# Kernel tuning notes

Hardware: AMD Instinct MI355X
Metric: run time of the kernel (lower is better)

## Reference

```python
import jax, jax.numpy as jnp
import numpy as np
from functools import partial

T, B, CH, H, W = 16, 4, 128, 128, 128
TAU, VTH, ALPHA, EPS = 2.0, 1.0, 2.0, 1e-5

# ATan surrogate-gradient spike (spikingjelly surrogate.ATan, alpha=2.0)
@jax.custom_vjp
def spike(x):
    return (x >= 0.0).astype(x.dtype)

def _spike_fwd(x):
    return spike(x), x

def _spike_bwd(x, g):
    return (g * (ALPHA / 2.0) / (1.0 + (jnp.pi / 2.0 * ALPHA * x) ** 2),)

spike.defvjp(_spike_fwd, _spike_bwd)

def _conv(x, w):  # x [N,C,H,W], w [O,I,3,3], padding=1 -> SAME
    return jax.lax.conv_general_dilated(x, w, (1, 1), 'SAME',
                                        dimension_numbers=('NCHW', 'OIHW', 'NCHW'))

def _bn(x, g, b, m, v):  # inference-mode BatchNorm2d, channel axis 1
    inv = g / jnp.sqrt(v + EPS)
    return x * inv[:, None, None] + (b - m * inv)[:, None, None]

def _pool(x):  # MaxPool2d(2,2), NCHW
    return jax.lax.reduce_window(x, -jnp.inf, jax.lax.max,
                                 (1, 1, 2, 2), (1, 1, 2, 2), 'VALID')

def _lif(xs):  # xs [T, ...]; LIFNode: tau=2, v_th=1, v_reset=0, decay_input, hard reset (detached)
    def step(v, x):
        v = v + (x - v) / TAU                      # charge
        s = spike(v - VTH)                         # fire (Heaviside fwd, ATan bwd)
        v = v * (1.0 - jax.lax.stop_gradient(s))   # detached hard reset to 0
        return v, s
    return jax.lax.scan(step, jnp.zeros_like(xs[0]), xs)[1]

def _block(xs, w, g, b, m, v):  # conv -> BN -> LIF -> maxpool, xs [T,B,C,H,W]
    t, bs = xs.shape[0], xs.shape[1]
    y = _bn(_conv(xs.reshape((t * bs,) + xs.shape[2:]), w), g, b, m, v)
    y = _lif(y.reshape((t, bs) + y.shape[1:]))
    y = _pool(y.reshape((t * bs,) + y.shape[2:]))
    return y.reshape((t, bs) + y.shape[1:])


def setup_inputs() -> dict:
    key = jax.random.key(0)
    ks = jax.random.split(key, 8)
    inp = {'x': jax.random.uniform(ks[0], (T, B, 2, H, W), jnp.float32)}
    fan_ins = [2 * 9, CH * 9, CH * 9, CH * 9]
    for i in range(4):
        cin = 2 if i == 0 else CH
        inp[f'w{i+1}'] = jax.random.normal(ks[i + 1], (CH, cin, 3, 3), jnp.float32) * np.sqrt(2.0 / fan_ins[i]).astype(np.float32)
        inp[f'g{i+1}'] = jnp.ones((CH,), jnp.float32)
        inp[f'b{i+1}'] = jnp.zeros((CH,), jnp.float32)
        inp[f'm{i+1}'] = jnp.zeros((CH,), jnp.float32)
        inp[f'v{i+1}'] = jnp.ones((CH,), jnp.float32)
    inp['wfc'] = jax.random.normal(ks[5], (10, CH * 8 * 8), jnp.float32) * np.sqrt(1.0 / (CH * 64)).astype(np.float32)
    inp['bfc'] = jnp.zeros((10,), jnp.float32)
    return inp


def reference(x, w1, g1, b1, m1, v1, w2, g2, b2, m2, v2,
              w3, g3, b3, m3, v3, w4, g4, b4, m4, v4, wfc, bfc):
    y = _block(x, w1, g1, b1, m1, v1)   # [T,B,CH,64,64]
    y = _block(y, w2, g2, b2, m2, v2)   # [T,B,CH,32,32]
    y = _block(y, w3, g3, b3, m3, v3)   # [T,B,CH,16,16]
    y = _block(y, w4, g4, b4, m4, v4)   # [T,B,CH,8,8]
    z = y.reshape(y.shape[0], y.shape[1], -1) @ wfc.T + bfc  # [T,B,10]
    return _lif(z)                       # output spike train [T,B,10]
```

## Files before the change

### kernel.cpp

```cpp
#include <hip/hip_runtime.h>
#include <hip/hip_bf16.h>
#include <math.h>

#define T_STEPS 16

typedef __attribute__((ext_vector_type(8))) short bf16x8;
typedef __attribute__((ext_vector_type(16))) float f32x16;

__global__ __launch_bounds__(256) void prep_w3_kernel(
    const float* __restrict__ w2, const float* __restrict__ w3,
    const float* __restrict__ w4, __hip_bfloat16* __restrict__ wp2,
    __hip_bfloat16* __restrict__ wp3, __hip_bfloat16* __restrict__ wp4) {
  const float* w = blockIdx.y == 0 ? w2 : (blockIdx.y == 1 ? w3 : w4);
  __hip_bfloat16* wp = blockIdx.y == 0 ? wp2 : (blockIdx.y == 1 ? wp3 : wp4);
  int idx = blockIdx.x * 256 + threadIdx.x;
  if (idx >= 147456) return;
  int co = idx / 1152, rem = idx - co * 1152;
  int ci = rem / 9, tap = rem - ci * 9;
  float x = w[idx];
  float h = (float)__float2bfloat16(x);
  float r1 = x - h;
  float m = (float)__float2bfloat16(r1);
  float r2 = r1 - m;
  size_t base = (((size_t)tap * 16 + (ci >> 3)) * 128 + co) * 8 + (ci & 7);
  const size_t SSZ = 147456;
  wp[base] = __float2bfloat16(h);
  wp[SSZ + base] = __float2bfloat16(m);
  wp[2 * SSZ + base] = __float2bfloat16(r2);
}

__global__ __launch_bounds__(192) void pad_x_kernel(const float* __restrict__ x,
                                                    float* __restrict__ xp) {
  const int plane = blockIdx.x;
  const int row = blockIdx.y;
  const int c = threadIdx.x;
  if (c < 132) {
    float v = 0.f;
    int gr = row - 1, gc = c - 1;
    if ((unsigned)gr < 128u && (unsigned)gc < 128u)
      v = x[(size_t)plane * 16384 + gr * 128 + gc];
    xp[((size_t)plane * 130 + row) * 132 + c] = v;
  }
}

__global__ __launch_bounds__(256) void layer1_kernel(
    const float* __restrict__ xp, const float* __restrict__ w,
    const float* __restrict__ gn, const float* __restrict__ bn,
    const float* __restrict__ mn, const float* __restrict__ vn,
    __hip_bfloat16* __restrict__ out) {
  const int tid = threadIdx.x;
  const int tile = blockIdx.x;
  const int ty0 = (tile >> 2) * 32, tx0 = (tile & 3) * 32;
  const int co0 = blockIdx.y * 4;
  const int b = blockIdx.z;
  const int qx2 = (tid & 15) * 2;
  const int qy2 = (tid >> 4) * 2;
  const int yq = ty0 + qy2;
  const int xq = tx0 + qx2;

  float wreg[2][9][4];
#pragma unroll
  for (int j = 0; j < 4; ++j)
#pragma unroll
    for (int ci = 0; ci < 2; ++ci)
#pragma unroll
      for (int tap = 0; tap < 9; ++tap)
        wreg[ci][tap][j] = w[(co0 + j) * 18 + ci * 9 + tap];

  float scale[4], shift[4];
#pragma unroll
  for (int j = 0; j < 4; ++j) {
    float inv = gn[co0 + j] / sqrtf(vn[co0 + j] + 1e-5f);
    scale[j] = inv;
    shift[j] = bn[co0 + j] - mn[co0 + j] * inv;
  }

  float vm[4][4];
#pragma unroll
  for (int j = 0; j < 4; ++j)
#pragma unroll
    for (int p = 0; p < 4; ++p) vm[j][p] = 0.f;

  for (int t = 0; t < T_STEPS; ++t) {
    const float* xpt = xp + (size_t)((t * 4 + b) * 2) * 17160;
    float iv[2][4][4];
#pragma unroll
    for (int ci = 0; ci < 2; ++ci)
#pragma unroll
      for (int r = 0; r < 4; ++r)
        *(float4*)&iv[ci][r][0] =
            *(const float4*)(xpt + (size_t)(ci * 130 + yq + r) * 132 + xq);

    float acc[4][4];
#pragma unroll
    for (int j = 0; j < 4; ++j)
#pragma unroll
      for (int p = 0; p < 4; ++p) acc[j][p] = 0.f;

#pragma unroll
    for (int ci = 0; ci < 2; ++ci)
#pragma unroll
      for (int tap = 0; tap < 9; ++tap) {
        const int dy = tap / 3, dx = tap - dy * 3;
#pragma unroll
        for (int sy = 0; sy < 2; ++sy)
#pragma unroll
          for (int sx = 0; sx < 2; ++sx) {
            float xin = iv[ci][sy + dy][sx + dx];
            acc[0][sy * 2 + sx] += wreg[ci][tap][0] * xin;
            acc[1][sy * 2 + sx] += wreg[ci][tap][1] * xin;
            acc[2][sy * 2 + sx] += wreg[ci][tap][2] * xin;
            acc[3][sy * 2 + sx] += wreg[ci][tap][3] * xin;
          }
      }

    const int py = (ty0 >> 1) + (tid >> 4);
    const int px = (tx0 >> 1) + (tid & 15);
    short4 pk;
    short* pks = (short*)&pk;
#pragma unroll
    for (int j = 0; j < 4; ++j) {
      float mx = -1e30f;
#pragma unroll
      for (int p = 0; p < 4; ++p) {
        float yv = acc[j][p] * scale[j] + shift[j];
        float nv = vm[j][p] + (yv - vm[j][p]) * 0.5f;
        mx = fmaxf(mx, nv);
        vm[j][p] = (nv >= 1.0f) ? 0.f : nv;
      }
      __hip_bfloat16 bv = __float2bfloat16(mx >= 1.0f ? 1.0f : 0.0f);
      pks[j] = *(short*)&bv;
    }
    *(short4*)(out + (((size_t)(t * 4 + b) * 64 + py) * 64 + px) * 128 + co0) = pk;
  }
}

template <int S>
__global__ __launch_bounds__(256) void conv32_tb2_kernel(
    const __hip_bfloat16* __restrict__ spk, const __hip_bfloat16* __restrict__ wp,
    float* __restrict__ pre, int tb_base) {
  constexpr int TILES_X = S / 8;
  const int tile = blockIdx.x;
  const int ty0 = (tile / TILES_X) * 16;
  const int tx0 = (tile % TILES_X) * 8;
  const int pair = blockIdx.z;
  const int tbl0 = pair * 2;
  const int tb0 = tb_base + tbl0;
  const int tid = threadIdx.x;
  const int lane = tid & 63;
  const int wv = tid >> 6;

  __shared__ uint4 At4[2][2880];

#pragma unroll
  for (int i = 0; i < 2; ++i) {
    const __hip_bfloat16* sp = spk + (size_t)(tb0 + i) * S * S * 128;
    for (int job = tid; job < 2880; job += 256) {
      int c8 = job & 15, r = job >> 4;
      int y = (r * 6554) >> 16;
      int xx = r - y * 10;
      int gy = ty0 - 1 + y, gx = tx0 - 1 + xx;
      uint4 v = make_uint4(0u, 0u, 0u, 0u);
      if ((unsigned)gy < (unsigned)S && (unsigned)gx < (unsigned)S)
        v = *(const uint4*)(sp + ((size_t)(gy * S + gx)) * 128 + c8 * 8);
      At4[i][(y * 10 + xx) * 16 + (c8 ^ (xx & 7))] = v;
    }
  }
  __syncthreads();

  const int l31 = lane & 31, hh = lane >> 5;
  const int co = wv * 32 + l31;
  const int ly = l31 >> 3, lx = lane & 7;
  const uint4* A0 = &At4[0][0];
  const uint4* A1 = &At4[1][0];

  f32x16 acc0[4], acc1[4];
#pragma unroll
  for (int m = 0; m < 4; ++m)
#pragma unroll
    for (int r = 0; r < 16; ++r) { acc0[m][r] = 0.f; acc1[m][r] = 0.f; }

  const short* wpb = (const short*)wp + (size_t)co * 8;

  for (int tap = 0; tap < 9; ++tap) {
    const int dy = tap / 3, dx = tap - dy * 3;
    const int xx = lx + dx;
    const int sx7 = xx & 7;
#pragma unroll
    for (int kk = 0; kk < 8; ++kk) {
      const int kc = kk * 2 + hh;
      bf16x8 a0[4], a1[4];
#pragma unroll
      for (int m = 0; m < 4; ++m) {
        const int slot = ((m * 4 + ly + dy) * 10 + xx) * 16 + (kc ^ sx7);
        a0[m] = *(const bf16x8*)(A0 + slot);
        a1[m] = *(const bf16x8*)(A1 + slot);
      }
#pragma unroll
      for (int s = 0; s < 3; ++s) {
        bf16x8 bfr = *(const bf16x8*)(wpb + ((size_t)(s * 9 + tap) * 16 + kc) * 1024);
#pragma unroll
        for (int m = 0; m < 4; ++m)
          acc0[m] = __builtin_amdgcn_mfma_f32_32x32x16_bf16(a0[m], bfr, acc0[m], 0, 0, 0);
#pragma unroll
        for (int m = 0; m < 4; ++m)
          acc1[m] = __builtin_amdgcn_mfma_f32_32x32x16_bf16(a1[m], bfr, acc1[m], 0, 0, 0);
      }
    }
  }

  float* po0 = pre + (size_t)tbl0 * S * S * 128 + co;
  float* po1 = pre + (size_t)(tbl0 + 1) * S * S * 128 + co;
#pragma unroll
  for (int m = 0; m < 4; ++m)
#pragma unroll
    for (int r = 0; r < 16; ++r) {
      int row = (r & 3) + 8 * (r >> 2) + 4 * hh;
      int p = m * 32 + row;
      size_t off = ((size_t)(ty0 + (p >> 3)) * S + tx0 + (p & 7)) * 128;
      po0[off] = acc0[m][r];
      po1[off] = acc1[m][r];
    }
}

template <int S>
__global__ __launch_bounds__(256) void conv32_kernel(
    const __hip_bfloat16* __restrict__ spk, const __hip_bfloat16* __restrict__ wp,
    float* __restrict__ pre, int t_base) {
  constexpr int TILES_X = S / 8;
  const int tile = blockIdx.x;
  const int ty0 = (tile / TILES_X) * 16;
  const int tx0 = (tile % TILES_X) * 8;
  const int tbl = blockIdx.z;
  const int tbg = t_base * 4 + tbl;
  const int tid = threadIdx.x;
  const int lane = tid & 63;
  const int wv = tid >> 6;

  __shared__ uint4 At4[2880];

  const __hip_bfloat16* sp = spk + (size_t)tbg * S * S * 128;
#pragma unroll
  for (int k = 0; k < 12; ++k) {
    int job = k * 256 + tid;
    if (job < 2880) {
      int c8 = job & 15, r = job >> 4;
      int y = (r * 6554) >> 16;
      int xx = r - y * 10;
      int gy = ty0 - 1 + y, gx = tx0 - 1 + xx;
      uint4 v = make_uint4(0u, 0u, 0u, 0u);
      if ((unsigned)gy < (unsigned)S && (unsigned)gx < (unsigned)S)
        v = *(const uint4*)(sp + ((size_t)(gy * S + gx)) * 128 + c8 * 8);
      At4[(y * 10 + xx) * 16 + (c8 ^ (xx & 7))] = v;
    }
  }
  __syncthreads();

  const int l31 = lane & 31, hh = lane >> 5;
  const int co = wv * 32 + l31;
  const int ly = l31 >> 3, lx = lane & 7;

  f32x16 acc[4];
#pragma unroll
  for (int m = 0; m < 4; ++m)
#pragma unroll
    for (int r = 0; r < 16; ++r) acc[m][r] = 0.f;

  const short* wpb = (const short*)wp + (size_t)co * 8;

  for (int tap = 0; tap < 9; ++tap) {
    const int dy = tap / 3, dx = tap - dy * 3;
    const int xx = lx + dx;
    const int sx7 = xx & 7;
#pragma unroll
    for (int kk = 0; kk < 8; ++kk) {
      const int kc = kk * 2 + hh;
      bf16x8 a[4];
#pragma unroll
      for (int m = 0; m < 4; ++m)
        a[m] = *(const bf16x8*)(At4 + ((m * 4 + ly + dy) * 10 + xx) * 16 + (kc ^ sx7));
#pragma unroll
      for (int s = 0; s < 3; ++s) {
        bf16x8 bfr = *(const bf16x8*)(wpb + ((size_t)(s * 9 + tap) * 16 + kc) * 1024);
#pragma unroll
        for (int m = 0; m < 4; ++m)
          acc[m] = __builtin_amdgcn_mfma_f32_32x32x16_bf16(a[m], bfr, acc[m], 0, 0, 0);
      }
    }
  }

  float* po = pre + (size_t)tbl * S * S * 128 + co;
#pragma unroll
  for (int m = 0; m < 4; ++m)
#pragma unroll
    for (int r = 0; r < 16; ++r) {
      int row = (r & 3) + 8 * (r >> 2) + 4 * hh;
      int p = m * 32 + row;
      po[((size_t)(ty0 + (p >> 3)) * S + tx0 + (p & 7)) * 128] = acc[m][r];
    }
}

template <int S>
__global__ __launch_bounds__(256) void lif_pool_kernel(
    const float* __restrict__ pre, __hip_bfloat16* __restrict__ spk,
    float* __restrict__ vm, const float* __restrict__ gn,
    const float* __restrict__ bn, const float* __restrict__ mn,
    const float* __restrict__ vn, int t_base, int nt) {
  constexpr int OS = S / 2, NQ = OS * OS;
  const int tid = threadIdx.x;
  const int co = tid & 127;
  const int q = blockIdx.x * 2 + (tid >> 7);
  const int b = blockIdx.z;
  const int qy = q / OS, qx = q - qy * OS;
  float inv = gn[co] / sqrtf(vn[co] + 1e-5f);
  float sc = inv, sh = bn[co] - mn[co] * inv;
  float* vp = vm + (((size_t)b * NQ + q) * 4) * 128 + co;
  float v0, v1, v2, v3;
  if (t_base == 0) {
    v0 = v1 = v2 = v3 = 0.f;
  } else {
    v0 = vp[0]; v1 = vp[128]; v2 = vp[256]; v3 = vp[384];
  }
  const size_t rowstride = (size_t)S * 128;
  for (int t = 0; t < nt; ++t) {
    const float* p = pre + (((size_t)(t * 4 + b) * S + qy * 2) * S + qx * 2) * 128 + co;
    float x00 = p[0] * sc + sh;
    float x01 = p[128] * sc + sh;
    float x10 = p[rowstride] * sc + sh;
    float x11 = p[rowstride + 128] * sc + sh;
    float n0 = v0 + (x00 - v0) * 0.5f; float s0 = n0 >= 1.f ? 1.f : 0.f; v0 = n0 >= 1.f ? 0.f : n0;
    float n1 = v1 + (x01 - v1) * 0.5f; float s1 = n1 >= 1.f ? 1.f : 0.f; v1 = n1 >= 1.f ? 0.f : n1;
    float n2 = v2 + (x10 - v2) * 0.5f; float s2 = n2 >= 1.f ? 1.f : 0.f; v2 = n2 >= 1.f ? 0.f : n2;
    float n3 = v3 + (x11 - v3) * 0.5f; float s3 = n3 >= 1.f ? 1.f : 0.f; v3 = n3 >= 1.f ? 0.f : n3;
    float pooled = fmaxf(fmaxf(s0, s1), fmaxf(s2, s3));
    spk[((size_t)((t_base + t) * 4 + b) * NQ + q) * 128 + co] = __float2bfloat16(pooled);
  }
  if (t_base + nt < T_STEPS) {
    vp[0] = v0; vp[128] = v1; vp[256] = v2; vp[384] = v3;
  }
}

__global__ __launch_bounds__(256) void fc_kernel(const __hip_bfloat16* __restrict__ a4,
                                                 const float* __restrict__ wfc,
                                                 const float* __restrict__ bfc,
                                                 float* __restrict__ z) {
  const int tb = blockIdx.x;
  const int tid = threadIdx.x;
  const __hip_bfloat16* a = a4 + (size_t)tb * 8192;
  float part[10];
#pragma unroll
  for (int o = 0; o < 10; ++o) part[o] = 0.f;
  for (int i = tid; i < 8192; i += 256) {
    int co = i >> 6, yx = i & 63;
    float av = __bfloat162float(a[yx * 128 + co]);
#pragma unroll
    for (int o = 0; o < 10; ++o) part[o] += av * wfc[o * 8192 + i];
  }
#pragma unroll
  for (int o = 0; o < 10; ++o)
    for (int off = 32; off > 0; off >>= 1) part[o] += __shfl_xor(part[o], off, 64);
  __shared__ float red[4][10];
  if ((tid & 63) == 0) {
#pragma unroll
    for (int o = 0; o < 10; ++o) red[tid >> 6][o] = part[o];
  }
  __syncthreads();
  if (tid < 10)
    z[tb * 10 + tid] = red[0][tid] + red[1][tid] + red[2][tid] + red[3][tid] + bfc[tid];
}

__global__ void out_lif_kernel(const float* __restrict__ z, float* __restrict__ out) {
  int i = threadIdx.x;
  if (i < 40) {
    float v = 0.f;
    for (int t = 0; t < T_STEPS; ++t) {
      float yv = z[t * 40 + i];
      float nv = v + (yv - v) * 0.5f;
      float s = (nv >= 1.0f) ? 1.0f : 0.0f;
      out[t * 40 + i] = s;
      v = (nv >= 1.0f) ? 0.f : nv;
    }
  }
}

extern "C" void kernel_launch(void* const* d_in, const int* in_sizes, int n_in,
                              void* d_out, int out_size, void* d_ws, size_t ws_size,
                              hipStream_t stream) {
  const float* x = (const float*)d_in[0];
  const float* w1 = (const float*)d_in[1];
  const float* g1 = (const float*)d_in[2];
  const float* b1 = (const float*)d_in[3];
  const float* m1 = (const float*)d_in[4];
  const float* v1 = (const float*)d_in[5];
  const float* w2 = (const float*)d_in[6];
  const float* g2 = (const float*)d_in[7];
  const float* b2 = (const float*)d_in[8];
  const float* m2 = (const float*)d_in[9];
  const float* v2 = (const float*)d_in[10];
  const float* w3 = (const float*)d_in[11];
  const float* g3 = (const float*)d_in[12];
  const float* b3 = (const float*)d_in[13];
  const float* m3 = (const float*)d_in[14];
  const float* v3 = (const float*)d_in[15];
  const float* w4 = (const float*)d_in[16];
  const float* g4 = (const float*)d_in[17];
  const float* b4 = (const float*)d_in[18];
  const float* m4 = (const float*)d_in[19];
  const float* v4 = (const float*)d_in[20];
  const float* wfc = (const float*)d_in[21];
  const float* bfc = (const float*)d_in[22];
  float* out = (float*)d_out;

  float* p = (float*)d_ws;
  __hip_bfloat16* wp2 = (__hip_bfloat16*)p; p += 221184;
  __hip_bfloat16* wp3 = (__hip_bfloat16*)p; p += 221184;
  __hip_bfloat16* wp4 = (__hip_bfloat16*)p; p += 221184;
  __hip_bfloat16* spk1 = (__hip_bfloat16*)p; p += 16777216;
  float* preH = p; p += 8388608;
  float* xp = preH;
  __hip_bfloat16* spk2 = (__hip_bfloat16*)p; p += 4194304;
  float* vm2 = p; p += 2097152;
  __hip_bfloat16* spk3 = (__hip_bfloat16*)p; p += 1048576;
  float* vm3 = p; p += 524288;
  __hip_bfloat16* spk4 = (__hip_bfloat16*)p; p += 262144;
  float* vm4 = p; p += 131072;
  float* z = p; p += 640;

  prep_w3_kernel<<<dim3(576, 3), 256, 0, stream>>>(w2, w3, w4, wp2, wp3, wp4);
  pad_x_kernel<<<dim3(128, 130), 192, 0, stream>>>(x, xp);

  layer1_kernel<<<dim3(16, 32, 4), 256, 0, stream>>>(xp, w1, g1, b1, m1, v1, spk1);

  for (int c = 0; c < 4; ++c) {
    conv32_tb2_kernel<64><<<dim3(32, 1, 8), 256, 0, stream>>>(spk1, wp2, preH, c * 16);
    lif_pool_kernel<64><<<dim3(512, 1, 4), 256, 0, stream>>>(preH, spk2, vm2, g2, b2,
                                                             m2, v2, c * 4, 4);
  }

  conv32_tb2_kernel<32><<<dim3(8, 1, 32), 256, 0, stream>>>(spk2, wp3, preH, 0);
  lif_pool_kernel<32><<<dim3(128, 1, 4), 256, 0, stream>>>(preH, spk3, vm3, g3, b3, m3, v3, 0, 16);

  conv32_kernel<16><<<dim3(2, 1, 64), 256, 0, stream>>>(spk3, wp4, preH, 0);
  lif_pool_kernel<16><<<dim3(32, 1, 4), 256, 0, stream>>>(preH, spk4, vm4, g4, b4, m4, v4, 0, 16);

  fc_kernel<<<64, 256, 0, stream>>>(spk4, wfc, bfc, z);
  out_lif_kernel<<<1, 64, 0, stream>>>(z, out);
}
```

Measured before the change: 519.7 us.

## Restructure conv blocks to share spike tiles across two channel halves

```diff
diff --git a/kernel.cpp b/kernel.cpp
--- a/kernel.cpp
+++ b/kernel.cpp
@@ -47,11 +47,11 @@
     const float* __restrict__ xp, const float* __restrict__ w,
     const float* __restrict__ gn, const float* __restrict__ bn,
     const float* __restrict__ mn, const float* __restrict__ vn,
-    __hip_bfloat16* __restrict__ out) {
+    __hip_bfloat16* __restrict__ out, int coBase) {
   const int tid = threadIdx.x;
   const int tile = blockIdx.x;
   const int ty0 = (tile >> 2) * 32, tx0 = (tile & 3) * 32;
-  const int co0 = blockIdx.y * 4;
+  const int co0 = coBase + blockIdx.y * 4;
   const int b = blockIdx.z;
   const int qx2 = (tid & 15) * 2;
   const int qy2 = (tid >> 4) * 2;
@@ -136,51 +136,47 @@
 }
 
 template <int S>
-__global__ __launch_bounds__(256) void conv32_tb2_kernel(
+__global__ __launch_bounds__(128) void conv32x2_kernel(
     const __hip_bfloat16* __restrict__ spk, const __hip_bfloat16* __restrict__ wp,
-    float* __restrict__ pre, int tb_base) {
+    float* __restrict__ pre, int t_base) {
   constexpr int TILES_X = S / 8;
   const int tile = blockIdx.x;
   const int ty0 = (tile / TILES_X) * 16;
   const int tx0 = (tile % TILES_X) * 8;
-  const int pair = blockIdx.z;
-  const int tbl0 = pair * 2;
-  const int tb0 = tb_base + tbl0;
+  const int tbl = blockIdx.z;
+  const int tbg = t_base * 4 + tbl;
   const int tid = threadIdx.x;
   const int lane = tid & 63;
   const int wv = tid >> 6;
 
-  __shared__ uint4 At4[2][2880];
-
-#pragma unroll
-  for (int i = 0; i < 2; ++i) {
-    const __hip_bfloat16* sp = spk + (size_t)(tb0 + i) * S * S * 128;
-    for (int job = tid; job < 2880; job += 256) {
-      int c8 = job & 15, r = job >> 4;
-      int y = (r * 6554) >> 16;
-      int xx = r - y * 10;
-      int gy = ty0 - 1 + y, gx = tx0 - 1 + xx;
-      uint4 v = make_uint4(0u, 0u, 0u, 0u);
-      if ((unsigned)gy < (unsigned)S && (unsigned)gx < (unsigned)S)
-        v = *(const uint4*)(sp + ((size_t)(gy * S + gx)) * 128 + c8 * 8);
-      At4[i][(y * 10 + xx) * 16 + (c8 ^ (xx & 7))] = v;
-    }
+  __shared__ uint4 At4[2880];
+
+  const __hip_bfloat16* sp = spk + (size_t)tbg * S * S * 128;
+  for (int job = tid; job < 2880; job += 128) {
+    int c8 = job & 15, r = job >> 4;
+    int y = (r * 6554) >> 16;
+    int xx = r - y * 10;
+    int gy = ty0 - 1 + y, gx = tx0 - 1 + xx;
+    uint4 v = make_uint4(0u, 0u, 0u, 0u);
+    if ((unsigned)gy < (unsigned)S && (unsigned)gx < (unsigned)S)
+      v = *(const uint4*)(sp + ((size_t)(gy * S + gx)) * 128 + c8 * 8);
+    At4[(y * 10 + xx) * 16 + (c8 ^ (xx & 7))] = v;
   }
   __syncthreads();
 
   const int l31 = lane & 31, hh = lane >> 5;
-  const int co = wv * 32 + l31;
+  const int coA = wv * 32 + l31;
+  const int coB = coA + 64;
   const int ly = l31 >> 3, lx = lane & 7;
-  const uint4* A0 = &At4[0][0];
-  const uint4* A1 = &At4[1][0];
-
-  f32x16 acc0[4], acc1[4];
+
+  f32x16 accA[4], accB[4];
 #pragma unroll
   for (int m = 0; m < 4; ++m)
 #pragma unroll
-    for (int r = 0; r < 16; ++r) { acc0[m][r] = 0.f; acc1[m][r] = 0.f; }
-
-  const short* wpb = (const short*)wp + (size_t)co * 8;
+    for (int r = 0; r < 16; ++r) { accA[m][r] = 0.f; accB[m][r] = 0.f; }
+
+  const short* wbA = (const short*)wp + (size_t)coA * 8;
+  const short* wbB = (const short*)wp + (size_t)coB * 8;
 
   for (int tap = 0; tap < 9; ++tap) {
     const int dy = tap / 3, dx = tap - dy * 3;
@@ -189,28 +185,27 @@
 #pragma unroll
     for (int kk = 0; kk < 8; ++kk) {
       const int kc = kk * 2 + hh;
-      bf16x8 a0[4], a1[4];
-#pragma unroll
-      for (int m = 0; m < 4; ++m) {
-        const int slot = ((m * 4 + ly + dy) * 10 + xx) * 16 + (kc ^ sx7);
-        a0[m] = *(const bf16x8*)(A0 + slot);
-        a1[m] = *(const bf16x8*)(A1 + slot);
+      bf16x8 a[4];
+#pragma unroll
+      for (int m = 0; m < 4; ++m)
+        a[m] = *(const bf16x8*)(At4 + ((m * 4 + ly + dy) * 10 + xx) * 16 + (kc ^ sx7));
+#pragma unroll
+      for (int s = 0; s < 3; ++s) {
+        const size_t woff = ((size_t)(s * 9 + tap) * 16 + kc) * 1024;
+        bf16x8 bA = *(const bf16x8*)(wbA + woff);
+        bf16x8 bB = *(const bf16x8*)(wbB + woff);
+#pragma unroll
+        for (int m = 0; m < 4; ++m)
+          accA[m] = __builtin_amdgcn_mfma_f32_32x32x16_bf16(a[m], bA, accA[m], 0, 0, 0);
+#pragma unroll
+        for (int m = 0; m < 4; ++m)
+          accB[m] = __builtin_amdgcn_mfma_f32_32x32x16_bf16(a[m], bB, accB[m], 0, 0, 0);
       }
-#pragma unroll
-      for (int s = 0; s < 3; ++s) {
-        bf16x8 bfr = *(const bf16x8*)(wpb + ((size_t)(s * 9 + tap) * 16 + kc) * 1024);
-#pragma unroll
-        for (int m = 0; m < 4; ++m)
-          acc0[m] = __builtin_amdgcn_mfma_f32_32x32x16_bf16(a0[m], bfr, acc0[m], 0, 0, 0);
-#pragma unroll
-        for (int m = 0; m < 4; ++m)
-          acc1[m] = __builtin_amdgcn_mfma_f32_32x32x16_bf16(a1[m], bfr, acc1[m], 0, 0, 0);
-      }
-    }
-  }
-
-  float* po0 = pre + (size_t)tbl0 * S * S * 128 + co;
-  float* po1 = pre + (size_t)(tbl0 + 1) * S * S * 128 + co;
+    }
+  }
+
+  float* poA = pre + (size_t)tbl * S * S * 128 + coA;
+  float* poB = pre + (size_t)tbl * S * S * 128 + coB;
 #pragma unroll
   for (int m = 0; m < 4; ++m)
 #pragma unroll
@@ -218,8 +213,8 @@
       int row = (r & 3) + 8 * (r >> 2) + 4 * hh;
       int p = m * 32 + row;
       size_t off = ((size_t)(ty0 + (p >> 3)) * S + tx0 + (p & 7)) * 128;
-      po0[off] = acc0[m][r];
-      po1[off] = acc1[m][r];
+      poA[off] = accA[m][r];
+      poB[off] = accB[m][r];
     }
 }
 
@@ -416,7 +411,7 @@
   __hip_bfloat16* wp3 = (__hip_bfloat16*)p; p += 221184;
   __hip_bfloat16* wp4 = (__hip_bfloat16*)p; p += 221184;
   __hip_bfloat16* spk1 = (__hip_bfloat16*)p; p += 16777216;
-  float* preH = p; p += 8388608;
+  float* preH = p; p += 16777216;
   float* xp = preH;
   __hip_bfloat16* spk2 = (__hip_bfloat16*)p; p += 4194304;
   float* vm2 = p; p += 2097152;
@@ -429,15 +424,15 @@
   prep_w3_kernel<<<dim3(576, 3), 256, 0, stream>>>(w2, w3, w4, wp2, wp3, wp4);
   pad_x_kernel<<<dim3(128, 130), 192, 0, stream>>>(x, xp);
 
-  layer1_kernel<<<dim3(16, 32, 4), 256, 0, stream>>>(xp, w1, g1, b1, m1, v1, spk1);
-
-  for (int c = 0; c < 4; ++c) {
-    conv32_tb2_kernel<64><<<dim3(32, 1, 8), 256, 0, stream>>>(spk1, wp2, preH, c * 16);
-    lif_pool_kernel<64><<<dim3(512, 1, 4), 256, 0, stream>>>(preH, spk2, vm2, g2, b2,
-                                                             m2, v2, c * 4, 4);
-  }
-
-  conv32_tb2_kernel<32><<<dim3(8, 1, 32), 256, 0, stream>>>(spk2, wp3, preH, 0);
+  layer1_kernel<<<dim3(16, 16, 4), 256, 0, stream>>>(xp, w1, g1, b1, m1, v1, spk1, 0);
+  layer1_kernel<<<dim3(16, 16, 4), 256, 0, stream>>>(xp, w1, g1, b1, m1, v1, spk1, 64);
+
+  conv32x2_kernel<64><<<dim3(32, 1, 32), 128, 0, stream>>>(spk1, wp2, preH, 0);
+  lif_pool_kernel<64><<<dim3(512, 1, 4), 256, 0, stream>>>(preH, spk2, vm2, g2, b2, m2, v2, 0, 8);
+  conv32x2_kernel<64><<<dim3(32, 1, 32), 128, 0, stream>>>(spk1, wp2, preH, 8);
+  lif_pool_kernel<64><<<dim3(512, 1, 4), 256, 0, stream>>>(preH, spk2, vm2, g2, b2, m2, v2, 8, 8);
+
+  conv32x2_kernel<32><<<dim3(8, 1, 64), 128, 0, stream>>>(spk2, wp3, preH, 0);
   lif_pool_kernel<32><<<dim3(128, 1, 4), 256, 0, stream>>>(preH, spk3, vm3, g3, b3, m3, v3, 0, 16);
 
   conv32_kernel<16><<<dim3(2, 1, 64), 256, 0, stream>>>(spk3, wp4, preH, 0);
```

Measured after the change: 640.2 us. 23.2% more time.
